# Optimization experiments

Hardware: AMD Instinct MI355X
Metric: run time of the kernel (lower is better)

Reference implementation:

```python
import jax, jax.numpy as jnp
import numpy as np

B, INF, OUTF, SEQ, FUT = 128, 64, 16, 512, 96
H, L = 512, 2
PROJ = INF - OUTF  # proj_size = 48 (PyTorch LSTM proj_size semantics)


def _cell(x, h, c, Wih, Whh, bih, bhh, Whr):
    # One LSTM-with-projection step; PyTorch gate order: i, f, g, o
    gates = x @ Wih.T + h @ Whh.T + bih + bhh  # (B, 4H)
    i, f, g, o = jnp.split(gates, 4, axis=-1)
    c = jax.nn.sigmoid(f) * c + jax.nn.sigmoid(i) * jnp.tanh(g)
    h = (jax.nn.sigmoid(o) * jnp.tanh(c)) @ Whr.T  # projected hidden (B, PROJ)
    return h, c


def _run_layer(xs, p):
    # xs: (T, B, F) time-major; returns (T, B, PROJ), final (h, c)
    Wih, Whh, bih, bhh, Whr = p
    bsz = xs.shape[1]
    h0 = jnp.zeros((bsz, PROJ), xs.dtype)
    c0 = jnp.zeros((bsz, H), xs.dtype)
    def step(carry, x_t):
        h, c = carry
        h, c = _cell(x_t, h, c, Wih, Whh, bih, bhh, Whr)
        return (h, c), h
    (hT, cT), hs = jax.lax.scan(step, (h0, c0), xs)
    return hs, hT, cT


def _encoder(x_btf, layers):
    xs = jnp.swapaxes(x_btf, 0, 1)  # (T, B, INF)
    hTs, cTs = [], []
    for p in layers:
        xs, hT, cT = _run_layer(xs, p)
        hTs.append(hT); cTs.append(cT)
    return jnp.swapaxes(xs, 0, 1), tuple(hTs), tuple(cTs)


def _decoder(h0s, c0s, first_prev, dec_btf, layers):
    xs = jnp.swapaxes(dec_btf, 0, 1)  # (FUT, B, OUTF)
    def step(carry, x_t):
        hs, cs, prev = carry
        inp = jnp.concatenate([prev, x_t], axis=-1)  # (B, INF)
        nh, nc = [], []
        for l, p in enumerate(layers):
            h, c = _cell(inp, hs[l], cs[l], *p)
            nh.append(h); nc.append(c)
            inp = h
        return (tuple(nh), tuple(nc), inp), inp
    _, preds = jax.lax.scan(step, (h0s, c0s, first_prev), xs)
    return jnp.swapaxes(preds, 0, 1)  # (B, FUT, PROJ)


def _forward(theta, insample_x_t, outsample_x_t, enc_layers, dec_layers):
    x = jnp.transpose(insample_x_t, (0, 2, 1))      # (B, SEQ, INF)
    dec = jnp.transpose(outsample_x_t, (0, 2, 1))   # (B, FUT, OUTF)
    backcast_seq, hTs, cTs = _encoder(x, enc_layers)  # (B, SEQ, PROJ)
    first_prev = x[:, -1, :PROJ]  # input_elements[:, -1, :-OUTF]
    preds = _decoder(hTs, cTs, first_prev, dec, dec_layers)  # (B, FUT, PROJ)
    backcast_basis = jnp.transpose(backcast_seq, (0, 2, 1))  # (B, PROJ, SEQ)
    forecast_basis = jnp.transpose(preds, (0, 2, 1))         # (B, PROJ, FUT)
    cut = forecast_basis.shape[1]
    backcast = jnp.einsum('bp,bpt->bt', theta[:, cut:], backcast_basis)
    forecast = jnp.einsum('bp,bpt->bt', theta[:, :cut], forecast_basis)
    return backcast, forecast


def setup_inputs() -> dict:
    key = jax.random.key(0)
    ks = iter(jax.random.split(key, 64))
    s = 1.0 / float(np.sqrt(H))
    def u(shape):
        return jax.random.uniform(next(ks), shape, jnp.float32, -s, s)
    inp = {
        "theta": jax.random.normal(next(ks), (B, 2 * PROJ), jnp.float32),
        "insample_x_t": jax.random.normal(next(ks), (B, INF, SEQ), jnp.float32),
        "outsample_x_t": jax.random.normal(next(ks), (B, OUTF, FUT), jnp.float32),
    }
    for net in ("enc", "dec"):
        for l in range(L):
            in_dim = INF if l == 0 else PROJ
            inp[f"{net}_Wih{l}"] = u((4 * H, in_dim))
            inp[f"{net}_Whh{l}"] = u((4 * H, PROJ))
            inp[f"{net}_bih{l}"] = u((4 * H,))
            inp[f"{net}_bhh{l}"] = u((4 * H,))
            inp[f"{net}_Whr{l}"] = u((PROJ, H))
    return inp


def reference(theta, insample_x_t, outsample_x_t,
              enc_Wih0, enc_Whh0, enc_bih0, enc_bhh0, enc_Whr0,
              enc_Wih1, enc_Whh1, enc_bih1, enc_bhh1, enc_Whr1,
              dec_Wih0, dec_Whh0, dec_bih0, dec_bhh0, dec_Whr0,
              dec_Wih1, dec_Whh1, dec_bih1, dec_bhh1, dec_Whr1):
    enc_layers = [(enc_Wih0, enc_Whh0, enc_bih0, enc_bhh0, enc_Whr0),
                  (enc_Wih1, enc_Whh1, enc_bih1, enc_bhh1, enc_Whr1)]
    dec_layers = [(dec_Wih0, dec_Whh0, dec_bih0, dec_bhh0, dec_Whr0),
                  (dec_Wih1, dec_Whh1, dec_bih1, dec_bhh1, dec_Whr1)]
    return _forward(theta, insample_x_t, outsample_x_t, enc_layers, dec_layers)
```

## Files before the change

kernel.cpp:

```cpp
#include <hip/hip_runtime.h>
#include <cstdint>
#include <cstddef>

#define BATCH 128
#define INF   64
#define OUTF  16
#define SEQ   512
#define FUT   96
#define HID   512
#define G4    2048
#define PROJ  48
#define ECH   4

#define DRG 8
#define DBG 8
#define DUP 64
#define DBP 16

typedef float f32x4 __attribute__((ext_vector_type(4)));

__device__ __forceinline__ float fsigmoid(float x) {
    float e = __builtin_amdgcn_exp2f(-1.4426950408889634f * x);
    return __builtin_amdgcn_rcpf(1.0f + e);
}
__device__ __forceinline__ float ftanh(float x) {
    float e = __builtin_amdgcn_exp2f(2.8853900817779268f * x);
    return 1.0f - 2.0f * __builtin_amdgcn_rcpf(1.0f + e);
}

__device__ __forceinline__ float gload(const float* p) {
    return __hip_atomic_load(p, __ATOMIC_RELAXED, __HIP_MEMORY_SCOPE_AGENT);
}
__device__ __forceinline__ void gstore(float* p, float v) {
    __hip_atomic_store(p, v, __ATOMIC_RELAXED, __HIP_MEMORY_SCOPE_AGENT);
}

__global__ void k_wtrans(const float* __restrict__ W, float* __restrict__ WT,
                         int R, int C) {
    __shared__ float tile[32][33];
    int r0 = blockIdx.x * 32, c0 = blockIdx.y * 32;
    int tx = threadIdx.x, ty = threadIdx.y;
    #pragma unroll
    for (int i = 0; i < 4; ++i) {
        int r = r0 + ty + 8 * i;
        if (r < R && c0 + tx < C) tile[ty + 8 * i][tx] = W[(size_t)r * C + c0 + tx];
    }
    __syncthreads();
    #pragma unroll
    for (int i = 0; i < 4; ++i) {
        int c = c0 + ty + 8 * i;
        if (c < C && r0 + tx < R) WT[(size_t)c * R + r0 + tx] = tile[tx][ty + 8 * i];
    }
}

__global__ __launch_bounds__(512)
__attribute__((amdgpu_waves_per_eu(2, 2)))
void k_enc(
    const float* __restrict__ x,
    const float* __restrict__ WT0, const float* __restrict__ Whh0,
    const float* __restrict__ bih0, const float* __restrict__ bhh0,
    const float* __restrict__ Whr0,
    const float* __restrict__ WT1, const float* __restrict__ Whh1,
    const float* __restrict__ bih1, const float* __restrict__ bhh1,
    const float* __restrict__ Whr1,
    float* __restrict__ H0x, float* __restrict__ H1,
    float* __restrict__ hs, float* __restrict__ cs,
    unsigned* __restrict__ eflags)
{
    const bool L1w = blockIdx.x >= BATCH;
    const int b = L1w ? blockIdx.x - BATCH : blockIdx.x;
    const int j = threadIdx.x;
    const int wave = j >> 6, lane = j & 63;
    const float* WT  = L1w ? WT1 : WT0;
    const float* Whh = L1w ? Whh1 : Whh0;
    const float* Whr = L1w ? Whr1 : Whr0;
    const float* bih = L1w ? bih1 : bih0;
    const float* bhh = L1w ? bhh1 : bhh0;
    const int K = L1w ? PROJ : INF;

    __shared__ float whr[PROJ][HID + 4];
    __shared__ __align__(16) float xs[ECH][INF + 4];
    __shared__ __align__(16) float ht_lds[HID];
    __shared__ __align__(16) float h_cur[PROJ];

    float wI[PROJ], wF[PROJ], wG[PROJ], wO[PROJ];
    #pragma unroll
    for (int k4 = 0; k4 < 12; ++k4) {
        float4 vi = *reinterpret_cast<const float4*>(&Whh[(size_t)j * PROJ + 4 * k4]);
        float4 vf = *reinterpret_cast<const float4*>(&Whh[(size_t)(j + HID) * PROJ + 4 * k4]);
        float4 vg = *reinterpret_cast<const float4*>(&Whh[(size_t)(j + 2 * HID) * PROJ + 4 * k4]);
        float4 vo = *reinterpret_cast<const float4*>(&Whh[(size_t)(j + 3 * HID) * PROJ + 4 * k4]);
        wI[4*k4+0]=vi.x; wI[4*k4+1]=vi.y; wI[4*k4+2]=vi.z; wI[4*k4+3]=vi.w;
        wF[4*k4+0]=vf.x; wF[4*k4+1]=vf.y; wF[4*k4+2]=vf.z; wF[4*k4+3]=vf.w;
        wG[4*k4+0]=vg.x; wG[4*k4+1]=vg.y; wG[4*k4+2]=vg.z; wG[4*k4+3]=vg.w;
        wO[4*k4+0]=vo.x; wO[4*k4+1]=vo.y; wO[4*k4+2]=vo.z; wO[4*k4+3]=vo.w;
    }
    for (int idx = j; idx < PROJ * HID; idx += 512) {
        int p = idx >> 9, jj = idx & 511;
        whr[p][jj] = Whr[(size_t)p * HID + jj];
    }
    float bI = bih[j] + bhh[j];
    float bF = bih[j + HID] + bhh[j + HID];
    float bG = bih[j + 2 * HID] + bhh[j + 2 * HID];
    float bO = bih[j + 3 * HID] + bhh[j + 3 * HID];
    float c = 0.f;
    if (j < PROJ) h_cur[j] = 0.f;
    __syncthreads();

    for (int t0 = 0; t0 < SEQ; t0 += ECH) {
        if (!L1w) {
            if (j < INF * ECH) {
                int k = j >> 2, dt = j & 3;
                xs[dt][k] = x[(size_t)b * INF * SEQ + (size_t)k * SEQ + t0 + dt];
            }
        } else {
            if (j == 0) {
                unsigned need = (unsigned)(t0 / ECH) + 1;
                while (__hip_atomic_load(&eflags[b * 16], __ATOMIC_RELAXED,
                                         __HIP_MEMORY_SCOPE_AGENT) < need)
                    __builtin_amdgcn_s_sleep(2);
            }
            __syncthreads();
            asm volatile("" ::: "memory");
            if (j < PROJ * ECH) {
                int dt = j / PROJ, p = j % PROJ;
                xs[dt][p] = gload(&H0x[((size_t)(t0 + dt) * BATCH + b) * PROJ + p]);
            }
        }
        __syncthreads();

        float a0[ECH], a1[ECH], a2[ECH], a3[ECH];
        #pragma unroll
        for (int dt = 0; dt < ECH; ++dt) { a0[dt] = bI; a1[dt] = bF; }
        for (int kq = 0; kq < K / 4; ++kq) {
            float wi0 = WT[(size_t)(kq*4+0) * G4 + j];
            float wi1 = WT[(size_t)(kq*4+1) * G4 + j];
            float wi2 = WT[(size_t)(kq*4+2) * G4 + j];
            float wi3 = WT[(size_t)(kq*4+3) * G4 + j];
            float wf0 = WT[(size_t)(kq*4+0) * G4 + HID + j];
            float wf1 = WT[(size_t)(kq*4+1) * G4 + HID + j];
            float wf2 = WT[(size_t)(kq*4+2) * G4 + HID + j];
            float wf3 = WT[(size_t)(kq*4+3) * G4 + HID + j];
            #pragma unroll
            for (int dt = 0; dt < ECH; ++dt) {
                float4 xv = *reinterpret_cast<const float4*>(&xs[dt][kq * 4]);
                a0[dt] += wi0*xv.x + wi1*xv.y + wi2*xv.z + wi3*xv.w;
                a1[dt] += wf0*xv.x + wf1*xv.y + wf2*xv.z + wf3*xv.w;
            }
        }
        #pragma unroll
        for (int dt = 0; dt < ECH; ++dt) { a2[dt] = bG; a3[dt] = bO; }
        for (int kq = 0; kq < K / 4; ++kq) {
            float wg0 = WT[(size_t)(kq*4+0) * G4 + 2 * HID + j];
            float wg1 = WT[(size_t)(kq*4+1) * G4 + 2 * HID + j];
            float wg2 = WT[(size_t)(kq*4+2) * G4 + 2 * HID + j];
            float wg3 = WT[(size_t)(kq*4+3) * G4 + 2 * HID + j];
            float wo0 = WT[(size_t)(kq*4+0) * G4 + 3 * HID + j];
            float wo1 = WT[(size_t)(kq*4+1) * G4 + 3 * HID + j];
            float wo2 = WT[(size_t)(kq*4+2) * G4 + 3 * HID + j];
            float wo3 = WT[(size_t)(kq*4+3) * G4 + 3 * HID + j];
            #pragma unroll
            for (int dt = 0; dt < ECH; ++dt) {
                float4 xv = *reinterpret_cast<const float4*>(&xs[dt][kq * 4]);
                a2[dt] += wg0*xv.x + wg1*xv.y + wg2*xv.z + wg3*xv.w;
                a3[dt] += wo0*xv.x + wo1*xv.y + wo2*xv.z + wo3*xv.w;
            }
        }

        #pragma unroll
        for (int dt = 0; dt < ECH; ++dt) {
            float ai = a0[dt], af = a1[dt], ag = a2[dt], ao = a3[dt];
            #pragma unroll
            for (int k4 = 0; k4 < 12; ++k4) {
                float4 h4 = *reinterpret_cast<const float4*>(&h_cur[4 * k4]);
                ai += wI[4*k4+0]*h4.x + wI[4*k4+1]*h4.y + wI[4*k4+2]*h4.z + wI[4*k4+3]*h4.w;
                af += wF[4*k4+0]*h4.x + wF[4*k4+1]*h4.y + wF[4*k4+2]*h4.z + wF[4*k4+3]*h4.w;
                ag += wG[4*k4+0]*h4.x + wG[4*k4+1]*h4.y + wG[4*k4+2]*h4.z + wG[4*k4+3]*h4.w;
                ao += wO[4*k4+0]*h4.x + wO[4*k4+1]*h4.y + wO[4*k4+2]*h4.z + wO[4*k4+3]*h4.w;
            }
            float si = fsigmoid(ai), sf = fsigmoid(af), so = fsigmoid(ao), tg = ftanh(ag);
            c = sf * c + si * tg;
            ht_lds[j] = so * ftanh(c);
            __syncthreads();
            float rq[6];
            #pragma unroll
            for (int q = 0; q < 6; ++q) {
                int p = wave * 6 + q;
                float s = 0.f;
                #pragma unroll
                for (int m = 0; m < 8; ++m)
                    s += whr[p][lane + 64 * m] * ht_lds[lane + 64 * m];
                #pragma unroll
                for (int o = 32; o; o >>= 1) s += __shfl_xor(s, o, 64);
                rq[q] = s;
            }
            if (lane == 0) {
                int t = t0 + dt;
                #pragma unroll
                for (int q = 0; q < 6; ++q) {
                    int p = wave * 6 + q;
                    float v = rq[q];
                    h_cur[p] = v;
                    if (!L1w) gstore(&H0x[((size_t)t * BATCH + b) * PROJ + p], v);
                    else      H1[((size_t)t * BATCH + b) * PROJ + p] = v;
                }
            }
            __syncthreads();
        }
        if (!L1w) {
            asm volatile("s_waitcnt vmcnt(0)" ::: "memory");
            __syncthreads();
            if (j == 0)
                __hip_atomic_store(&eflags[b * 16], (unsigned)(t0 / ECH) + 1,
                                   __ATOMIC_RELAXED, __HIP_MEMORY_SCOPE_AGENT);
        }
    }
    cs[((size_t)(L1w ? BATCH : 0) + b) * HID + j] = c;
    if (j < PROJ) hs[((size_t)(L1w ? BATCH : 0) + b) * PROJ + j] = h_cur[j];
}

__global__ __launch_bounds__(512) void k_decA(
    const float* __restrict__ xdec,
    const float* __restrict__ Wih0, const float* __restrict__ Whh0,
    const float* __restrict__ bih0, const float* __restrict__ bhh0,
    const float* __restrict__ Whr0,
    const float* __restrict__ hs, float* __restrict__ cs0,
    const float* __restrict__ xin,
    const float* __restrict__ PPa_r, float* __restrict__ PPa_w,
    const float* __restrict__ PPb_r, float* __restrict__ PRED, int t)
{
    const int bg = blockIdx.x & 7, rg = blockIdx.x >> 3;
    const int tid = threadIdx.x;
    const int kq = tid & 3, rhalf = tid >> 2;
    const int u2 = tid >> 3, b2 = tid & 7;
    const int uglob = rg * DUP + u2;
    const int w = tid >> 6, lane = tid & 63;
    const size_t PSTR = (size_t)BATCH * PROJ;

    __shared__ __align__(16) float inp0[DBP][120];
    __shared__ float xch[4][DUP][17];
    __shared__ float htl[DBP][68];
    __shared__ float wslT0[DUP][52];

    for (int i = tid; i < PROJ * DUP; i += 512) {
        int p = i >> 6, uu = i & 63;
        wslT0[uu][p] = Whr0[(size_t)p * HID + rg * DUP + uu];
    }
    float bs0[4];
    #pragma unroll
    for (int gg = 0; gg < 4; ++gg)
        bs0[gg] = bih0[gg * HID + uglob] + bhh0[gg * HID + uglob];
    float c0[2];
    #pragma unroll
    for (int hh = 0; hh < 2; ++hh)
        c0[hh] = cs0[(size_t)(bg * DBP + b2 + 8 * hh) * HID + uglob];

    if (t == 0) {
        for (int i = tid; i < DBP * PROJ; i += 512) {
            int b = i / PROJ, p = i % PROJ;
            int bglob = bg * DBP + b;
            inp0[b][p]      = hs[(size_t)bglob * PROJ + p];
            inp0[b][48 + p] = xin[(size_t)bglob * INF * SEQ + (size_t)p * SEQ + (SEQ - 1)];
        }
        if (tid < DBP * OUTF) {
            int b = tid >> 4, f = tid & 15;
            inp0[b][96 + f] = xdec[(size_t)(bg * DBP + b) * (OUTF * FUT) + (size_t)f * FUT];
        }
    } else {
        if (tid < 192) {
            int b = tid / 12, p = (tid % 12) * 4;
            int bglob = bg * DBP + b;
            f32x4 s = {0.f, 0.f, 0.f, 0.f};
            #pragma unroll
            for (int rr = 0; rr < DRG; ++rr)
                s += *reinterpret_cast<const f32x4*>(&PPa_r[(size_t)rr * PSTR + (size_t)bglob * PROJ + p]);
            *reinterpret_cast<f32x4*>(&inp0[b][p]) = s;
        } else if (tid < 384) {
            int idx = tid - 192;
            int b = idx / 12, p = (idx % 12) * 4;
            int bglob = bg * DBP + b;
            f32x4 s = {0.f, 0.f, 0.f, 0.f};
            #pragma unroll
            for (int rr = 0; rr < DRG; ++rr)
                s += *reinterpret_cast<const f32x4*>(&PPb_r[(size_t)rr * PSTR + (size_t)bglob * PROJ + p]);
            *reinterpret_cast<f32x4*>(&inp0[b][48 + p]) = s;
            if (rg == 0)
                *reinterpret_cast<f32x4*>(&PRED[((size_t)(t - 1) * BATCH + bglob) * PROJ + p]) = s;
        } else {
            #pragma unroll
            for (int rep = 0; rep < 2; ++rep) {
                int i2 = (tid - 384) + rep * 128;
                int b = i2 >> 4, f = i2 & 15;
                inp0[b][96 + f] = xdec[(size_t)(bg * DBP + b) * (OUTF * FUT) + (size_t)f * FUT + t];
            }
        }
    }
    __syncthreads();

    #pragma unroll
    for (int p = 0; p < 2; ++p) {
        int rid = p * 128 + rhalf;
        int g = rid >> 6, u = rid & 63;
        int grow = g * HID + rg * DUP + u;
        float wv[28];
        #pragma unroll
        for (int kk = 0; kk < 28; ++kk) {
            int k = kq * 28 + kk;
            wv[kk] = (k < 48) ? Whh0[(size_t)grow * 48 + k]
                              : Wih0[(size_t)grow * 64 + (k - 48)];
        }
        float acc[DBP];
        #pragma unroll
        for (int b = 0; b < DBP; ++b) acc[b] = 0.f;
        const float* srcA = &inp0[0][0] + kq * 28;
        #pragma unroll
        for (int i4 = 0; i4 < 7; ++i4) {
            float w0 = wv[i4*4], w1 = wv[i4*4+1], w2 = wv[i4*4+2], w3 = wv[i4*4+3];
            #pragma unroll
            for (int b = 0; b < DBP; ++b) {
                float4 xv = *reinterpret_cast<const float4*>(&srcA[b * 120 + i4 * 4]);
                acc[b] += w0*xv.x + w1*xv.y + w2*xv.z + w3*xv.w;
            }
        }
        #pragma unroll
        for (int b = 0; b < DBP; ++b) {
            acc[b] += __shfl_xor(acc[b], 1, 64);
            acc[b] += __shfl_xor(acc[b], 2, 64);
        }
        if (kq == 0) {
            #pragma unroll
            for (int b = 0; b < DBP; ++b) xch[g][u][b] = acc[b];
        }
    }
    __syncthreads();
    #pragma unroll
    for (int hh = 0; hh < 2; ++hh) {
        int b = b2 + 8 * hh;
        float gi = xch[0][u2][b] + bs0[0];
        float gf = xch[1][u2][b] + bs0[1];
        float gc = xch[2][u2][b] + bs0[2];
        float go = xch[3][u2][b] + bs0[3];
        float si = fsigmoid(gi), sf = fsigmoid(gf), so = fsigmoid(go), tg = ftanh(gc);
        c0[hh] = sf * c0[hh] + si * tg;
        htl[b][u2] = so * ftanh(c0[hh]);
        cs0[(size_t)(bg * DBP + b) * HID + uglob] = c0[hh];
    }
    __syncthreads();
    if (lane < PROJ) {
        #pragma unroll
        for (int bb = 0; bb < 2; ++bb) {
            int b = 2 * w + bb;
            float s = 0.f;
            #pragma unroll
            for (int u4 = 0; u4 < 16; ++u4) {
                float4 hv = *reinterpret_cast<const float4*>(&htl[b][u4 * 4]);
                s += wslT0[u4*4+0][lane]*hv.x + wslT0[u4*4+1][lane]*hv.y
                   + wslT0[u4*4+2][lane]*hv.z + wslT0[u4*4+3][lane]*hv.w;
            }
            PPa_w[(size_t)rg * PSTR + (size_t)(bg * DBP + b) * PROJ + lane] = s;
        }
    }
}

__global__ __launch_bounds__(512) void k_decB(
    const float* __restrict__ Wih1, const float* __restrict__ Whh1,
    const float* __restrict__ bih1, const float* __restrict__ bhh1,
    const float* __restrict__ Whr1,
    const float* __restrict__ hs, float* __restrict__ cs1,
    const float* __restrict__ PPa_r, const float* __restrict__ PPb_r,
    float* __restrict__ PPb_w, int t)
{
    const int bg = blockIdx.x & 7, rg = blockIdx.x >> 3;
    const int tid = threadIdx.x;
    const int kq = tid & 3, rhalf = tid >> 2;
    const int u2 = tid >> 3, b2 = tid & 7;
    const int uglob = rg * DUP + u2;
    const int w = tid >> 6, lane = tid & 63;
    const size_t PSTR = (size_t)BATCH * PROJ;

    __shared__ __align__(16) float h0n[DBP][52];
    __shared__ __align__(16) float h1b[DBP][52];
    __shared__ float xch[4][DUP][17];
    __shared__ float htl[DBP][68];
    __shared__ float wslT1[DUP][52];

    for (int i = tid; i < PROJ * DUP; i += 512) {
        int p = i >> 6, uu = i & 63;
        wslT1[uu][p] = Whr1[(size_t)p * HID + rg * DUP + uu];
    }
    float bs1[4];
    #pragma unroll
    for (int gg = 0; gg < 4; ++gg)
        bs1[gg] = bih1[gg * HID + uglob] + bhh1[gg * HID + uglob];
    float c1[2];
    #pragma unroll
    for (int hh = 0; hh < 2; ++hh)
        c1[hh] = cs1[(size_t)(bg * DBP + b2 + 8 * hh) * HID + uglob];

    if (tid < 192) {
        int b = tid / 12, p = (tid % 12) * 4;
        int bglob = bg * DBP + b;
        f32x4 s = {0.f, 0.f, 0.f, 0.f};
        #pragma unroll
        for (int rr = 0; rr < DRG; ++rr)
            s += *reinterpret_cast<const f32x4*>(&PPa_r[(size_t)rr * PSTR + (size_t)bglob * PROJ + p]);
        *reinterpret_cast<f32x4*>(&h0n[b][p]) = s;
    } else if (tid < 384) {
        int idx = tid - 192;
        int b = idx / 12, p = (idx % 12) * 4;
        int bglob = bg * DBP + b;
        if (t == 0) {
            f32x4 s = *reinterpret_cast<const f32x4*>(&hs[(size_t)(BATCH + bglob) * PROJ + p]);
            *reinterpret_cast<f32x4*>(&h1b[b][p]) = s;
        } else {
            f32x4 s = {0.f, 0.f, 0.f, 0.f};
            #pragma unroll
            for (int rr = 0; rr < DRG; ++rr)
                s += *reinterpret_cast<const f32x4*>(&PPb_r[(size_t)rr * PSTR + (size_t)bglob * PROJ + p]);
            *reinterpret_cast<f32x4*>(&h1b[b][p]) = s;
        }
    }
    __syncthreads();

    #pragma unroll
    for (int p = 0; p < 2; ++p) {
        int rid = p * 128 + rhalf;
        int g = rid >> 6, u = rid & 63;
        int grow = g * HID + rg * DUP + u;
        float wv[24];
        #pragma unroll
        for (int kk = 0; kk < 24; ++kk) {
            int k = kq * 24 + kk;
            wv[kk] = (k < 48) ? Whh1[(size_t)grow * 48 + k]
                              : Wih1[(size_t)grow * 48 + (k - 48)];
        }
        const float* srcB = (kq < 2) ? (&h1b[0][0] + kq * 24)
                                     : (&h0n[0][0] + (kq - 2) * 24);
        float acc[DBP];
        #pragma unroll
        for (int b = 0; b < DBP; ++b) acc[b] = 0.f;
        #pragma unroll
        for (int i4 = 0; i4 < 6; ++i4) {
            float w0 = wv[i4*4], w1 = wv[i4*4+1], w2 = wv[i4*4+2], w3 = wv[i4*4+3];
            #pragma unroll
            for (int b = 0; b < DBP; ++b) {
                float4 xv = *reinterpret_cast<const float4*>(&srcB[b * 52 + i4 * 4]);
                acc[b] += w0*xv.x + w1*xv.y + w2*xv.z + w3*xv.w;
            }
        }
        #pragma unroll
        for (int b = 0; b < DBP; ++b) {
            acc[b] += __shfl_xor(acc[b], 1, 64);
            acc[b] += __shfl_xor(acc[b], 2, 64);
        }
        if (kq == 0) {
            #pragma unroll
            for (int b = 0; b < DBP; ++b) xch[g][u][b] = acc[b];
        }
    }
    __syncthreads();
    #pragma unroll
    for (int hh = 0; hh < 2; ++hh) {
        int b = b2 + 8 * hh;
        float gi = xch[0][u2][b] + bs1[0];
        float gf = xch[1][u2][b] + bs1[1];
        float gc = xch[2][u2][b] + bs1[2];
        float go = xch[3][u2][b] + bs1[3];
        float si = fsigmoid(gi), sf = fsigmoid(gf), so = fsigmoid(go), tg = ftanh(gc);
        c1[hh] = sf * c1[hh] + si * tg;
        htl[b][u2] = so * ftanh(c1[hh]);
        cs1[(size_t)(bg * DBP + b) * HID + uglob] = c1[hh];
    }
    __syncthreads();
    if (lane < PROJ) {
        #pragma unroll
        for (int bb = 0; bb < 2; ++bb) {
            int b = 2 * w + bb;
            float s = 0.f;
            #pragma unroll
            for (int u4 = 0; u4 < 16; ++u4) {
                float4 hv = *reinterpret_cast<const float4*>(&htl[b][u4 * 4]);
                s += wslT1[u4*4+0][lane]*hv.x + wslT1[u4*4+1][lane]*hv.y
                   + wslT1[u4*4+2][lane]*hv.z + wslT1[u4*4+3][lane]*hv.w;
            }
            PPb_w[(size_t)rg * PSTR + (size_t)(bg * DBP + b) * PROJ + lane] = s;
        }
    }
}

__global__ void k_predlast(const float* __restrict__ PPb_r, float* __restrict__ PRED) {
    int b = blockIdx.x;
    int p = threadIdx.x;
    if (p < PROJ) {
        const size_t PSTR = (size_t)BATCH * PROJ;
        float s = 0.f;
        #pragma unroll
        for (int rr = 0; rr < DRG; ++rr)
            s += PPb_r[(size_t)rr * PSTR + (size_t)b * PROJ + p];
        PRED[((size_t)(FUT - 1) * BATCH + b) * PROJ + p] = s;
    }
}

__global__ void k_final(const float* __restrict__ theta, const float* __restrict__ H1,
                        const float* __restrict__ PRED, float* __restrict__ out)
{
    int b = blockIdx.x;
    __shared__ float th[2 * PROJ];
    if (threadIdx.x < 2 * PROJ) th[threadIdx.x] = theta[(size_t)b * 2 * PROJ + threadIdx.x];
    __syncthreads();
    for (int t = threadIdx.x; t < SEQ; t += 256) {
        float s = 0.f;
        #pragma unroll
        for (int p = 0; p < PROJ; ++p) s += th[PROJ + p] * H1[((size_t)t * BATCH + b) * PROJ + p];
        out[(size_t)b * SEQ + t] = s;
    }
    for (int t = threadIdx.x; t < FUT; t += 256) {
        float s = 0.f;
        #pragma unroll
        for (int p = 0; p < PROJ; ++p) s += th[p] * PRED[((size_t)t * BATCH + b) * PROJ + p];
        out[(size_t)BATCH * SEQ + (size_t)b * FUT + t] = s;
    }
}

extern "C" void kernel_launch(void* const* d_in, const int* in_sizes, int n_in,
                              void* d_out, int out_size, void* d_ws, size_t ws_size,
                              hipStream_t stream)
{
    (void)in_sizes; (void)n_in; (void)out_size; (void)ws_size;
    const float* theta = (const float*)d_in[0];
    const float* xin   = (const float*)d_in[1];
    const float* xdec  = (const float*)d_in[2];
    const float* eW0i = (const float*)d_in[3];
    const float* eW0h = (const float*)d_in[4];
    const float* eb0i = (const float*)d_in[5];
    const float* eb0h = (const float*)d_in[6];
    const float* eW0r = (const float*)d_in[7];
    const float* eW1i = (const float*)d_in[8];
    const float* eW1h = (const float*)d_in[9];
    const float* eb1i = (const float*)d_in[10];
    const float* eb1h = (const float*)d_in[11];
    const float* eW1r = (const float*)d_in[12];
    const float* dW0i = (const float*)d_in[13];
    const float* dW0h = (const float*)d_in[14];
    const float* db0i = (const float*)d_in[15];
    const float* db0h = (const float*)d_in[16];
    const float* dW0r = (const float*)d_in[17];
    const float* dW1i = (const float*)d_in[18];
    const float* dW1h = (const float*)d_in[19];
    const float* db1i = (const float*)d_in[20];
    const float* db1h = (const float*)d_in[21];
    const float* dW1r = (const float*)d_in[22];

    float* ws = (float*)d_ws;
    size_t off = 0;
    float* H0x  = ws + off; off += (size_t)SEQ * BATCH * PROJ;
    float* H1   = ws + off; off += (size_t)SEQ * BATCH * PROJ;
    float* PRED = ws + off; off += (size_t)FUT * BATCH * PROJ;
    float* hs   = ws + off; off += (size_t)2 * BATCH * PROJ;
    float* cs   = ws + off; off += (size_t)2 * BATCH * HID;
    float* WT0  = ws + off; off += (size_t)INF * G4;
    float* WT1  = ws + off; off += (size_t)PROJ * G4;
    const size_t DPP = (size_t)DRG * BATCH * PROJ;
    float* PPa  = ws + off; off += 2 * DPP;
    float* PPb  = ws + off; off += 2 * DPP;
    off = (off + 63) & ~(size_t)63;
    unsigned* eflags = (unsigned*)(ws + off); off += BATCH * 16;

    float* cs0 = cs;
    float* cs1 = cs + (size_t)BATCH * HID;

    hipMemsetAsync(eflags, 0, BATCH * 16 * sizeof(unsigned), stream);
    k_wtrans<<<dim3(G4 / 32, 2), dim3(32, 8), 0, stream>>>(eW0i, WT0, G4, INF);
    k_wtrans<<<dim3(G4 / 32, 2), dim3(32, 8), 0, stream>>>(eW1i, WT1, G4, PROJ);
    k_enc<<<2 * BATCH, 512, 0, stream>>>(xin,
                                         WT0, eW0h, eb0i, eb0h, eW0r,
                                         WT1, eW1h, eb1i, eb1h, eW1r,
                                         H0x, H1, hs, cs, eflags);

    for (int t = 0; t < FUT; ++t) {
        const float* ppaR = PPa + (size_t)((t - 1) & 1) * DPP;
        float*       ppaW = PPa + (size_t)(t & 1) * DPP;
        const float* ppbR = PPb + (size_t)((t - 1) & 1) * DPP;
        float*       ppbW = PPb + (size_t)(t & 1) * DPP;
        k_decA<<<DRG * DBG, 512, 0, stream>>>(xdec, dW0i, dW0h, db0i, db0h, dW0r,
                                              hs, cs0, xin, ppaR, ppaW, ppbR, PRED, t);
        k_decB<<<DRG * DBG, 512, 0, stream>>>(dW1i, dW1h, db1i, db1h, dW1r,
                                              hs, cs1, ppaW, ppbR, ppbW, t);
    }
    k_predlast<<<BATCH, 64, 0, stream>>>(PPb + (size_t)((FUT - 1) & 1) * DPP, PRED);
    k_final<<<BATCH, 256, 0, stream>>>(theta, H1, PRED, (float*)d_out);
}
```

Baseline: 5.239 ms.

## Process two batch rows per encoder block and interleave input weights by k-quad

The encoder kernel now assigns two batch rows to each block (128 blocks instead of 256), so each weight load from Wih, Whh and Whr is reused across two sequences. The input-weight transpose is replaced by a k-quad interleaved layout that allows one 16-byte vector load per gate. The recurrent Whh weights are no longer cached in registers but streamed from global memory/cache every step, and the waves_per_eu attribute is dropped. This halves the block count and lengthens each block's serial chain. It also adds per-step global reads of Whh, in exchange for lower register pressure and shared weight traffic.

Result: slower. 8.668 ms (+65.5%).

```diff
diff --git a/kernel.cpp b/kernel.cpp
--- a/kernel.cpp
+++ b/kernel.cpp
@@ -35,43 +35,37 @@
     __hip_atomic_store(p, v, __ATOMIC_RELAXED, __HIP_MEMORY_SCOPE_AGENT);
 }
 
-__global__ void k_wtrans(const float* __restrict__ W, float* __restrict__ WT,
-                         int R, int C) {
-    __shared__ float tile[32][33];
-    int r0 = blockIdx.x * 32, c0 = blockIdx.y * 32;
-    int tx = threadIdx.x, ty = threadIdx.y;
-    #pragma unroll
-    for (int i = 0; i < 4; ++i) {
-        int r = r0 + ty + 8 * i;
-        if (r < R && c0 + tx < C) tile[ty + 8 * i][tx] = W[(size_t)r * C + c0 + tx];
-    }
-    __syncthreads();
-    #pragma unroll
-    for (int i = 0; i < 4; ++i) {
-        int c = c0 + ty + 8 * i;
-        if (c < C && r0 + tx < R) WT[(size_t)c * R + r0 + tx] = tile[tx][ty + 8 * i];
-    }
-}
-
-__global__ __launch_bounds__(512)
-__attribute__((amdgpu_waves_per_eu(2, 2)))
-void k_enc(
+__global__ void k_wtrans4(const float* __restrict__ W, float* __restrict__ WT4, int K) {
+    int idx = blockIdx.x * 256 + threadIdx.x;
+    int nkq = K / 4;
+    if (idx >= G4 * nkq) return;
+    int row = idx & (G4 - 1);
+    int kq  = idx >> 11;
+    f32x4 v;
+    v.x = W[(size_t)row * K + kq * 4 + 0];
+    v.y = W[(size_t)row * K + kq * 4 + 1];
+    v.z = W[(size_t)row * K + kq * 4 + 2];
+    v.w = W[(size_t)row * K + kq * 4 + 3];
+    *reinterpret_cast<f32x4*>(&WT4[(size_t)idx * 4]) = v;
+}
+
+__global__ __launch_bounds__(512) void k_enc(
     const float* __restrict__ x,
-    const float* __restrict__ WT0, const float* __restrict__ Whh0,
+    const float* __restrict__ WT4_0, const float* __restrict__ Whh0,
     const float* __restrict__ bih0, const float* __restrict__ bhh0,
     const float* __restrict__ Whr0,
-    const float* __restrict__ WT1, const float* __restrict__ Whh1,
+    const float* __restrict__ WT4_1, const float* __restrict__ Whh1,
     const float* __restrict__ bih1, const float* __restrict__ bhh1,
     const float* __restrict__ Whr1,
     float* __restrict__ H0x, float* __restrict__ H1,
     float* __restrict__ hs, float* __restrict__ cs,
     unsigned* __restrict__ eflags)
 {
-    const bool L1w = blockIdx.x >= BATCH;
-    const int b = L1w ? blockIdx.x - BATCH : blockIdx.x;
+    const bool L1w = blockIdx.x >= 64;
+    const int pr = blockIdx.x & 63;
     const int j = threadIdx.x;
     const int wave = j >> 6, lane = j & 63;
-    const float* WT  = L1w ? WT1 : WT0;
+    const float* WT4 = L1w ? WT4_1 : WT4_0;
     const float* Whh = L1w ? Whh1 : Whh0;
     const float* Whr = L1w ? Whr1 : Whr0;
     const float* bih = L1w ? bih1 : bih0;
@@ -79,22 +73,10 @@
     const int K = L1w ? PROJ : INF;
 
     __shared__ float whr[PROJ][HID + 4];
-    __shared__ __align__(16) float xs[ECH][INF + 4];
-    __shared__ __align__(16) float ht_lds[HID];
-    __shared__ __align__(16) float h_cur[PROJ];
-
-    float wI[PROJ], wF[PROJ], wG[PROJ], wO[PROJ];
-    #pragma unroll
-    for (int k4 = 0; k4 < 12; ++k4) {
-        float4 vi = *reinterpret_cast<const float4*>(&Whh[(size_t)j * PROJ + 4 * k4]);
-        float4 vf = *reinterpret_cast<const float4*>(&Whh[(size_t)(j + HID) * PROJ + 4 * k4]);
-        float4 vg = *reinterpret_cast<const float4*>(&Whh[(size_t)(j + 2 * HID) * PROJ + 4 * k4]);
-        float4 vo = *reinterpret_cast<const float4*>(&Whh[(size_t)(j + 3 * HID) * PROJ + 4 * k4]);
-        wI[4*k4+0]=vi.x; wI[4*k4+1]=vi.y; wI[4*k4+2]=vi.z; wI[4*k4+3]=vi.w;
-        wF[4*k4+0]=vf.x; wF[4*k4+1]=vf.y; wF[4*k4+2]=vf.z; wF[4*k4+3]=vf.w;
-        wG[4*k4+0]=vg.x; wG[4*k4+1]=vg.y; wG[4*k4+2]=vg.z; wG[4*k4+3]=vg.w;
-        wO[4*k4+0]=vo.x; wO[4*k4+1]=vo.y; wO[4*k4+2]=vo.z; wO[4*k4+3]=vo.w;
-    }
+    __shared__ __align__(16) float xs[2][ECH][INF + 4];
+    __shared__ __align__(16) float ht_lds[2][HID];
+    __shared__ __align__(16) float h_cur[2][PROJ];
+
     for (int idx = j; idx < PROJ * HID; idx += 512) {
         int p = idx >> 9, jj = idx & 511;
         whr[p][jj] = Whr[(size_t)p * HID + jj];
@@ -103,106 +85,122 @@
     float bF = bih[j + HID] + bhh[j + HID];
     float bG = bih[j + 2 * HID] + bhh[j + 2 * HID];
     float bO = bih[j + 3 * HID] + bhh[j + 3 * HID];
-    float c = 0.f;
-    if (j < PROJ) h_cur[j] = 0.f;
-    __syncthreads();
+    float c2[2] = {0.f, 0.f};
+    if (j < 2 * PROJ) h_cur[j / PROJ][j % PROJ] = 0.f;
+    __syncthreads();
+
+    const float* w0p = Whh + (size_t)j * PROJ;
 
     for (int t0 = 0; t0 < SEQ; t0 += ECH) {
         if (!L1w) {
-            if (j < INF * ECH) {
-                int k = j >> 2, dt = j & 3;
-                xs[dt][k] = x[(size_t)b * INF * SEQ + (size_t)k * SEQ + t0 + dt];
+            {
+                int b = j >> 8, rem = j & 255, k = rem >> 2, dt = rem & 3;
+                xs[b][dt][k] = x[(size_t)(2 * pr + b) * INF * SEQ + (size_t)k * SEQ + t0 + dt];
             }
         } else {
             if (j == 0) {
                 unsigned need = (unsigned)(t0 / ECH) + 1;
-                while (__hip_atomic_load(&eflags[b * 16], __ATOMIC_RELAXED,
+                while (__hip_atomic_load(&eflags[pr * 16], __ATOMIC_RELAXED,
                                          __HIP_MEMORY_SCOPE_AGENT) < need)
                     __builtin_amdgcn_s_sleep(2);
             }
             __syncthreads();
             asm volatile("" ::: "memory");
-            if (j < PROJ * ECH) {
-                int dt = j / PROJ, p = j % PROJ;
-                xs[dt][p] = gload(&H0x[((size_t)(t0 + dt) * BATCH + b) * PROJ + p]);
+            if (j < 2 * PROJ * ECH) {
+                int b = j / (PROJ * ECH), rem = j % (PROJ * ECH);
+                int dt = rem / PROJ, p = rem % PROJ;
+                xs[b][dt][p] = gload(&H0x[((size_t)(t0 + dt) * BATCH + 2 * pr + b) * PROJ + p]);
             }
         }
         __syncthreads();
 
-        float a0[ECH], a1[ECH], a2[ECH], a3[ECH];
-        #pragma unroll
-        for (int dt = 0; dt < ECH; ++dt) { a0[dt] = bI; a1[dt] = bF; }
+        float a0[ECH][2], a1[ECH][2], a2[ECH][2], a3[ECH][2];
+        #pragma unroll
+        for (int dt = 0; dt < ECH; ++dt)
+            #pragma unroll
+            for (int b = 0; b < 2; ++b) {
+                a0[dt][b] = bI; a1[dt][b] = bF; a2[dt][b] = bG; a3[dt][b] = bO;
+            }
         for (int kq = 0; kq < K / 4; ++kq) {
-            float wi0 = WT[(size_t)(kq*4+0) * G4 + j];
-            float wi1 = WT[(size_t)(kq*4+1) * G4 + j];
-            float wi2 = WT[(size_t)(kq*4+2) * G4 + j];
-            float wi3 = WT[(size_t)(kq*4+3) * G4 + j];
-            float wf0 = WT[(size_t)(kq*4+0) * G4 + HID + j];
-            float wf1 = WT[(size_t)(kq*4+1) * G4 + HID + j];
-            float wf2 = WT[(size_t)(kq*4+2) * G4 + HID + j];
-            float wf3 = WT[(size_t)(kq*4+3) * G4 + HID + j];
-            #pragma unroll
-            for (int dt = 0; dt < ECH; ++dt) {
-                float4 xv = *reinterpret_cast<const float4*>(&xs[dt][kq * 4]);
-                a0[dt] += wi0*xv.x + wi1*xv.y + wi2*xv.z + wi3*xv.w;
-                a1[dt] += wf0*xv.x + wf1*xv.y + wf2*xv.z + wf3*xv.w;
-            }
-        }
-        #pragma unroll
-        for (int dt = 0; dt < ECH; ++dt) { a2[dt] = bG; a3[dt] = bO; }
-        for (int kq = 0; kq < K / 4; ++kq) {
-            float wg0 = WT[(size_t)(kq*4+0) * G4 + 2 * HID + j];
-            float wg1 = WT[(size_t)(kq*4+1) * G4 + 2 * HID + j];
-            float wg2 = WT[(size_t)(kq*4+2) * G4 + 2 * HID + j];
-            float wg3 = WT[(size_t)(kq*4+3) * G4 + 2 * HID + j];
-            float wo0 = WT[(size_t)(kq*4+0) * G4 + 3 * HID + j];
-            float wo1 = WT[(size_t)(kq*4+1) * G4 + 3 * HID + j];
-            float wo2 = WT[(size_t)(kq*4+2) * G4 + 3 * HID + j];
-            float wo3 = WT[(size_t)(kq*4+3) * G4 + 3 * HID + j];
-            #pragma unroll
-            for (int dt = 0; dt < ECH; ++dt) {
-                float4 xv = *reinterpret_cast<const float4*>(&xs[dt][kq * 4]);
-                a2[dt] += wg0*xv.x + wg1*xv.y + wg2*xv.z + wg3*xv.w;
-                a3[dt] += wo0*xv.x + wo1*xv.y + wo2*xv.z + wo3*xv.w;
-            }
+            f32x4 wi = *reinterpret_cast<const f32x4*>(&WT4[((size_t)kq * G4 + j) * 4]);
+            f32x4 wf = *reinterpret_cast<const f32x4*>(&WT4[((size_t)kq * G4 + HID + j) * 4]);
+            f32x4 wg = *reinterpret_cast<const f32x4*>(&WT4[((size_t)kq * G4 + 2 * HID + j) * 4]);
+            f32x4 wo = *reinterpret_cast<const f32x4*>(&WT4[((size_t)kq * G4 + 3 * HID + j) * 4]);
+            #pragma unroll
+            for (int b = 0; b < 2; ++b)
+                #pragma unroll
+                for (int dt = 0; dt < ECH; ++dt) {
+                    f32x4 xv = *reinterpret_cast<const f32x4*>(&xs[b][dt][kq * 4]);
+                    a0[dt][b] += wi.x*xv.x + wi.y*xv.y + wi.z*xv.z + wi.w*xv.w;
+                    a1[dt][b] += wf.x*xv.x + wf.y*xv.y + wf.z*xv.z + wf.w*xv.w;
+                    a2[dt][b] += wg.x*xv.x + wg.y*xv.y + wg.z*xv.z + wg.w*xv.w;
+                    a3[dt][b] += wo.x*xv.x + wo.y*xv.y + wo.z*xv.z + wo.w*xv.w;
+                }
         }
 
         #pragma unroll
         for (int dt = 0; dt < ECH; ++dt) {
-            float ai = a0[dt], af = a1[dt], ag = a2[dt], ao = a3[dt];
+            float ai[2], af[2], ag[2], ao[2];
+            #pragma unroll
+            for (int b = 0; b < 2; ++b) {
+                ai[b] = a0[dt][b]; af[b] = a1[dt][b];
+                ag[b] = a2[dt][b]; ao[b] = a3[dt][b];
+            }
             #pragma unroll
             for (int k4 = 0; k4 < 12; ++k4) {
-                float4 h4 = *reinterpret_cast<const float4*>(&h_cur[4 * k4]);
-                ai += wI[4*k4+0]*h4.x + wI[4*k4+1]*h4.y + wI[4*k4+2]*h4.z + wI[4*k4+3]*h4.w;
-                af += wF[4*k4+0]*h4.x + wF[4*k4+1]*h4.y + wF[4*k4+2]*h4.z + wF[4*k4+3]*h4.w;
-                ag += wG[4*k4+0]*h4.x + wG[4*k4+1]*h4.y + wG[4*k4+2]*h4.z + wG[4*k4+3]*h4.w;
-                ao += wO[4*k4+0]*h4.x + wO[4*k4+1]*h4.y + wO[4*k4+2]*h4.z + wO[4*k4+3]*h4.w;
-            }
-            float si = fsigmoid(ai), sf = fsigmoid(af), so = fsigmoid(ao), tg = ftanh(ag);
-            c = sf * c + si * tg;
-            ht_lds[j] = so * ftanh(c);
+                f32x4 wi = *reinterpret_cast<const f32x4*>(w0p + 4 * k4);
+                f32x4 wf = *reinterpret_cast<const f32x4*>(w0p + (size_t)HID * PROJ + 4 * k4);
+                f32x4 wg = *reinterpret_cast<const f32x4*>(w0p + (size_t)2 * HID * PROJ + 4 * k4);
+                f32x4 wo = *reinterpret_cast<const f32x4*>(w0p + (size_t)3 * HID * PROJ + 4 * k4);
+                #pragma unroll
+                for (int b = 0; b < 2; ++b) {
+                    f32x4 h4 = *reinterpret_cast<const f32x4*>(&h_cur[b][4 * k4]);
+                    ai[b] += wi.x*h4.x + wi.y*h4.y + wi.z*h4.z + wi.w*h4.w;
+                    af[b] += wf.x*h4.x + wf.y*h4.y + wf.z*h4.z + wf.w*h4.w;
+                    ag[b] += wg.x*h4.x + wg.y*h4.y + wg.z*h4.z + wg.w*h4.w;
+                    ao[b] += wo.x*h4.x + wo.y*h4.y + wo.z*h4.z + wo.w*h4.w;
+                }
+            }
+            #pragma unroll
+            for (int b = 0; b < 2; ++b) {
+                float si = fsigmoid(ai[b]), sf = fsigmoid(af[b]);
+                float so = fsigmoid(ao[b]), tg = ftanh(ag[b]);
+                c2[b] = sf * c2[b] + si * tg;
+                ht_lds[b][j] = so * ftanh(c2[b]);
+            }
             __syncthreads();
-            float rq[6];
+            float r0[6], r1[6];
             #pragma unroll
             for (int q = 0; q < 6; ++q) {
                 int p = wave * 6 + q;
-                float s = 0.f;
+                float s0 = 0.f, s1 = 0.f;
                 #pragma unroll
-                for (int m = 0; m < 8; ++m)
-                    s += whr[p][lane + 64 * m] * ht_lds[lane + 64 * m];
+                for (int m = 0; m < 8; ++m) {
+                    float wv = whr[p][lane + 64 * m];
+                    s0 += wv * ht_lds[0][lane + 64 * m];
+                    s1 += wv * ht_lds[1][lane + 64 * m];
+                }
                 #pragma unroll
-                for (int o = 32; o; o >>= 1) s += __shfl_xor(s, o, 64);
-                rq[q] = s;
+                for (int o = 32; o; o >>= 1) {
+                    s0 += __shfl_xor(s0, o, 64);
+                    s1 += __shfl_xor(s1, o, 64);
+                }
+                r0[q] = s0; r1[q] = s1;
             }
             if (lane == 0) {
                 int t = t0 + dt;
                 #pragma unroll
                 for (int q = 0; q < 6; ++q) {
                     int p = wave * 6 + q;
-                    float v = rq[q];
-                    h_cur[p] = v;
-                    if (!L1w) gstore(&H0x[((size_t)t * BATCH + b) * PROJ + p], v);
-                    else      H1[((size_t)t * BATCH + b) * PROJ + p] = v;
+                    h_cur[0][p] = r0[q];
+                    h_cur[1][p] = r1[q];
+                    if (!L1w) {
+                        gstore(&H0x[((size_t)t * BATCH + 2 * pr) * PROJ + p], r0[q]);
+                        gstore(&H0x[((size_t)t * BATCH + 2 * pr + 1) * PROJ + p], r1[q]);
+                    } else {
+                        H1[((size_t)t * BATCH + 2 * pr) * PROJ + p] = r0[q];
+                        H1[((size_t)t * BATCH + 2 * pr + 1) * PROJ + p] = r1[q];
+                    }
                 }
             }
             __syncthreads();
@@ -211,12 +209,17 @@
             asm volatile("s_waitcnt vmcnt(0)" ::: "memory");
             __syncthreads();
             if (j == 0)
-                __hip_atomic_store(&eflags[b * 16], (unsigned)(t0 / ECH) + 1,
+                __hip_atomic_store(&eflags[pr * 16], (unsigned)(t0 / ECH) + 1,
                                    __ATOMIC_RELAXED, __HIP_MEMORY_SCOPE_AGENT);
         }
     }
-    cs[((size_t)(L1w ? BATCH : 0) + b) * HID + j] = c;
-    if (j < PROJ) hs[((size_t)(L1w ? BATCH : 0) + b) * PROJ + j] = h_cur[j];
+    #pragma unroll
+    for (int b = 0; b < 2; ++b)
+        cs[((size_t)(L1w ? BATCH : 0) + 2 * pr + b) * HID + j] = c2[b];
+    if (j < 2 * PROJ) {
+        int b = j / PROJ, p = j % PROJ;
+        hs[((size_t)(L1w ? BATCH : 0) + 2 * pr + b) * PROJ + p] = h_cur[b][p];
+    }
 }
 
 __global__ __launch_bounds__(512) void k_decA(
@@ -558,24 +561,24 @@
     float* PRED = ws + off; off += (size_t)FUT * BATCH * PROJ;
     float* hs   = ws + off; off += (size_t)2 * BATCH * PROJ;
     float* cs   = ws + off; off += (size_t)2 * BATCH * HID;
-    float* WT0  = ws + off; off += (size_t)INF * G4;
-    float* WT1  = ws + off; off += (size_t)PROJ * G4;
+    float* WT4_0 = ws + off; off += (size_t)INF * G4;
+    float* WT4_1 = ws + off; off += (size_t)PROJ * G4;
     const size_t DPP = (size_t)DRG * BATCH * PROJ;
     float* PPa  = ws + off; off += 2 * DPP;
     float* PPb  = ws + off; off += 2 * DPP;
     off = (off + 63) & ~(size_t)63;
-    unsigned* eflags = (unsigned*)(ws + off); off += BATCH * 16;
+    unsigned* eflags = (unsigned*)(ws + off); off += 64 * 16;
 
     float* cs0 = cs;
     float* cs1 = cs + (size_t)BATCH * HID;
 
-    hipMemsetAsync(eflags, 0, BATCH * 16 * sizeof(unsigned), stream);
-    k_wtrans<<<dim3(G4 / 32, 2), dim3(32, 8), 0, stream>>>(eW0i, WT0, G4, INF);
-    k_wtrans<<<dim3(G4 / 32, 2), dim3(32, 8), 0, stream>>>(eW1i, WT1, G4, PROJ);
-    k_enc<<<2 * BATCH, 512, 0, stream>>>(xin,
-                                         WT0, eW0h, eb0i, eb0h, eW0r,
-                                         WT1, eW1h, eb1i, eb1h, eW1r,
-                                         H0x, H1, hs, cs, eflags);
+    hipMemsetAsync(eflags, 0, 64 * 16 * sizeof(unsigned), stream);
+    k_wtrans4<<<(G4 * (INF / 4) + 255) / 256, 256, 0, stream>>>(eW0i, WT4_0, INF);
+    k_wtrans4<<<(G4 * (PROJ / 4) + 255) / 256, 256, 0, stream>>>(eW1i, WT4_1, PROJ);
+    k_enc<<<128, 512, 0, stream>>>(xin,
+                                   WT4_0, eW0h, eb0i, eb0h, eW0r,
+                                   WT4_1, eW1h, eb1i, eb1h, eW1r,
+                                   H0x, H1, hs, cs, eflags);
 
     for (int t = 0; t < FUT; ++t) {
         const float* ppaR = PPa + (size_t)((t - 1) & 1) * DPP;
```
